# Optimization experiments

Hardware: AMD Instinct MI355X
Metric: run time of the kernel (lower is better)

The kernel has to match this reference:

```python
import jax, jax.numpy as jnp
import numpy as np

N = 50000          # nodes
E = 800000         # random edges (self-loops added in reference, per PyG default)
B = 64             # graphs in batch
IN_DIM = 773
HID = 256
OUT = 128
H1, D1 = 4, 64     # heads, head_dim layer 1 (256 = 4*64)
H2, D2 = 4, 32     # heads, head_dim layer 2 (128 = 4*32)
NEG_SLOPE = 0.2


def setup_inputs() -> dict:
    key = jax.random.key(0)
    ks = jax.random.split(key, 20)
    s = 0.02
    x = jax.random.normal(ks[0], (N, IN_DIM), dtype=jnp.float32)
    edge_index = jax.random.randint(ks[1], (2, E), 0, N, dtype=jnp.int32)
    batch = jnp.sort(jax.random.randint(ks[2], (N,), 0, B, dtype=jnp.int32))
    return {
        "x": x,
        "edge_index": edge_index,
        "batch": batch,
        "W_in": jax.random.normal(ks[3], (IN_DIM, HID), jnp.float32) * s,
        "b_in": jnp.zeros((HID,), jnp.float32),
        "W1": jax.random.normal(ks[4], (HID, H1 * D1), jnp.float32) * s,
        "att_src1": jax.random.normal(ks[5], (H1, D1), jnp.float32) * s,
        "att_dst1": jax.random.normal(ks[6], (H1, D1), jnp.float32) * s,
        "b1": jnp.zeros((H1 * D1,), jnp.float32),
        "W2": jax.random.normal(ks[7], (HID, H2 * D2), jnp.float32) * s,
        "att_src2": jax.random.normal(ks[8], (H2, D2), jnp.float32) * s,
        "att_dst2": jax.random.normal(ks[9], (H2, D2), jnp.float32) * s,
        "b2": jnp.zeros((H2 * D2,), jnp.float32),
        "W_cls": jax.random.normal(ks[10], (OUT, 2), jnp.float32) * s,
        "b_cls": jnp.zeros((2,), jnp.float32),
        "W_conf": jax.random.normal(ks[11], (OUT, 1), jnp.float32) * s,
        "b_conf": jnp.zeros((1,), jnp.float32),
    }


def _gat_layer(h, src, dst, W, att_src, att_dst, bias, heads, dim):
    # h: (N, F_in). PyG GATConv, concat=True, eval mode (dropout off).
    hW = (h @ W).reshape(N, heads, dim)                    # (N, H, D)
    a_src = jnp.einsum("nhd,hd->nh", hW, att_src)          # (N, H)
    a_dst = jnp.einsum("nhd,hd->nh", hW, att_dst)
    e = a_src[src] + a_dst[dst]                            # (E', H)
    e = jax.nn.leaky_relu(e, NEG_SLOPE)
    # segment softmax over incoming edges of each dst node
    m = jax.ops.segment_max(e, dst, num_segments=N)        # (N, H)
    ex = jnp.exp(e - m[dst])
    z = jax.ops.segment_sum(ex, dst, num_segments=N)       # (N, H)
    alpha = ex / (z[dst] + 1e-16)                          # (E', H)
    msg = hW[src] * alpha[:, :, None]                      # (E', H, D)
    out = jax.ops.segment_sum(msg, dst, num_segments=N)    # (N, H, D)
    return out.reshape(N, heads * dim) + bias


def reference(x, edge_index, batch, W_in, b_in,
              W1, att_src1, att_dst1, b1,
              W2, att_src2, att_dst2, b2,
              W_cls, b_cls, W_conf, b_conf):
    loops = jnp.arange(N, dtype=edge_index.dtype)
    src = jnp.concatenate([edge_index[0], loops])
    dst = jnp.concatenate([edge_index[1], loops])

    h = jax.nn.relu(x @ W_in + b_in)                       # (N, 256)
    h = jax.nn.relu(_gat_layer(h, src, dst, W1, att_src1, att_dst1, b1, H1, D1))
    h = _gat_layer(h, src, dst, W2, att_src2, att_dst2, b2, H2, D2)
    h = jax.nn.relu(h)                                     # (N, 128)

    # global mean pool over graphs
    sums = jax.ops.segment_sum(h, batch, num_segments=B)   # (B, 128)
    cnts = jax.ops.segment_sum(jnp.ones((N,), h.dtype), batch, num_segments=B)
    graph_emb = sums / jnp.maximum(cnts, 1.0)[:, None]

    class_logits = graph_emb @ W_cls + b_cls               # (B, 2)
    confidence = jax.nn.sigmoid(graph_emb @ W_conf + b_conf)  # (B, 1)
    return class_logits, confidence
```

## Files before the change

kernel.cpp:

```cpp
#include <hip/hip_runtime.h>
#include <math.h>

#define NN 50000
#define NE 800000
#define NB 64
#define IND 773
#define MPAD 50048
#define SCAN_B 196

typedef __attribute__((ext_vector_type(8))) short short8_t;
typedef __attribute__((ext_vector_type(4))) float f32x4;
typedef __attribute__((ext_vector_type(2))) float f32x2;

__device__ __forceinline__ float lrelu(float x) { return x > 0.f ? x : 0.2f * x; }
__device__ __forceinline__ short f2b(float f) {
    unsigned u = __float_as_uint(f);
    unsigned r = (u + 0x7fffu + ((u >> 16) & 1u)) >> 16;
    return (short)r;
}
__device__ __forceinline__ float b2f(short s) {
    return __uint_as_float(((unsigned)(unsigned short)s) << 16);
}
__device__ __forceinline__ unsigned char enc8(float v) {
    return (unsigned char)(__builtin_amdgcn_cvt_pk_fp8_f32(v, v, 0, false) & 0xff);
}
__device__ __forceinline__ void dec4(unsigned w, float* v) {
    f32x2 lo = __builtin_amdgcn_cvt_pk_f32_fp8((int)w, false);
    f32x2 hi = __builtin_amdgcn_cvt_pk_f32_fp8((int)w, true);
    v[0] = lo[0]; v[1] = lo[1]; v[2] = hi[0]; v[3] = hi[1];
}
__device__ __forceinline__ void dec2(unsigned w, float* v) {
    f32x2 lo = __builtin_amdgcn_cvt_pk_f32_fp8((int)w, false);
    v[0] = lo[0]; v[1] = lo[1];
}

#define GLOAD16(g, l) __builtin_amdgcn_global_load_lds(                         \
    (const __attribute__((address_space(1))) void*)(g),                         \
    (__attribute__((address_space(3))) void*)(l), 16, 0, 0)

__global__ __launch_bounds__(512) void gemm_a(const float* __restrict__ X,
                                              const short* __restrict__ Bt,
                                              const float* __restrict__ bias,
                                              short* __restrict__ C) {
    const int K = 800, N = 256, NT = 25;
    __shared__ short As[2][128 * 32];
    __shared__ short Bs[2][256 * 32];
    const int t = threadIdx.x;
    const int w = t >> 6, l = t & 63;
    const int l15 = l & 15, lh = l >> 4;
    const int bm = blockIdx.x * 128;
    const int wr = (w >> 2) * 64, wc = (w & 3) * 64;
    const int arow = t >> 2, acb = (t & 3) * 8;
    const int gm = bm + arow;
    const bool rowok = gm < NN;
    const float* xrow = X + (size_t)gm * IND;
    const short* bG = Bt + (size_t)(t >> 2) * K + (t & 3) * 8;

    f32x4 acc[4][4];
#pragma unroll
    for (int i = 0; i < 4; ++i)
#pragma unroll
        for (int j = 0; j < 4; ++j) acc[i][j] = (f32x4){0.f, 0.f, 0.f, 0.f};

    short8_t rA;
    auto loadA = [&](int it) {
        int gk = it * 32 + acb;
        if (rowok && gk + 7 < IND) {
            float4 v0 = *(const float4*)(xrow + gk);
            float4 v1 = *(const float4*)(xrow + gk + 4);
            rA[0] = f2b(v0.x); rA[1] = f2b(v0.y); rA[2] = f2b(v0.z); rA[3] = f2b(v0.w);
            rA[4] = f2b(v1.x); rA[5] = f2b(v1.y); rA[6] = f2b(v1.z); rA[7] = f2b(v1.w);
        } else {
#pragma unroll
            for (int j = 0; j < 8; ++j)
                rA[j] = (rowok && gk + j < IND) ? f2b(xrow[gk + j]) : (short)0;
        }
    };
    auto stageB = [&](int buf, int it) {
        GLOAD16(bG + it * 32, &Bs[buf][w * 512]);
        GLOAD16(bG + (size_t)128 * K + it * 32, &Bs[buf][128 * 32 + w * 512]);
    };

    loadA(0);
    stageB(0, 0);
    stageB(1, 1);
    *(short8_t*)&As[0][arow * 32 + acb] = rA;
    loadA(1);
    __syncthreads();

    for (int it = 0; it < NT; ++it) {
        const int c = it & 1, n = c ^ 1;
        short8_t af[4], bfr[4];
#pragma unroll
        for (int mi = 0; mi < 4; ++mi)
            af[mi] = *(const short8_t*)&As[c][(wr + mi * 16 + l15) * 32 + lh * 8];
#pragma unroll
        for (int ni = 0; ni < 4; ++ni)
            bfr[ni] = *(const short8_t*)&Bs[c][(wc + ni * 16 + l15) * 32 + lh * 8];
        if (it + 1 < NT) *(short8_t*)&As[n][arow * 32 + acb] = rA;
#pragma unroll
        for (int mi = 0; mi < 4; ++mi)
#pragma unroll
            for (int ni = 0; ni < 4; ++ni)
                acc[mi][ni] = __builtin_amdgcn_mfma_f32_16x16x32_bf16(af[mi], bfr[ni], acc[mi][ni], 0, 0, 0);
        __syncthreads();
        if (it + 2 < NT) {
            loadA(it + 2);
            stageB(c, it + 2);
        }
    }

#pragma unroll
    for (int mi = 0; mi < 4; ++mi) {
#pragma unroll
        for (int r = 0; r < 4; ++r) {
            int grow = bm + wr + mi * 16 + lh * 4 + r;
            if (grow >= NN) continue;
#pragma unroll
            for (int ni = 0; ni < 4; ++ni) {
                int gcol = wc + ni * 16 + l15;
                float v = fmaxf(acc[mi][ni][r] + bias[gcol], 0.f);
                C[(size_t)grow * N + gcol] = f2b(v);
            }
        }
    }
}

__global__ __launch_bounds__(256) void gemm_b(const short* __restrict__ A,
                                              const short* __restrict__ Bt,
                                              const float* __restrict__ att_s,
                                              const float* __restrict__ att_d,
                                              unsigned char* __restrict__ C8,
                                              float* __restrict__ a_s,
                                              float* __restrict__ a_d) {
    const int K = 256, N = 256, NT = 8;
    __shared__ short As[2][128 * 32];
    __shared__ short Bs[2][128 * 32];
    const int t = threadIdx.x;
    const int w = t >> 6, l = t & 63;
    const int l15 = l & 15, lh = l >> 4;
    const int bm = blockIdx.x * 128, bn = blockIdx.y * 128;
    const int wr = (w >> 1) * 64, wc = (w & 1) * 64;

    const short* aG = A + (size_t)(bm + w * 32 + (l >> 2)) * K + (l & 3) * 8;
    const short* bG = Bt + (size_t)(bn + w * 32 + (l >> 2)) * K + (l & 3) * 8;

    auto stage = [&](int buf, int k0) {
        GLOAD16(aG + k0, As[buf] + (w * 32) * 32);
        GLOAD16(aG + (size_t)16 * K + k0, As[buf] + (w * 32 + 16) * 32);
        GLOAD16(bG + k0, Bs[buf] + (w * 32) * 32);
        GLOAD16(bG + (size_t)16 * K + k0, Bs[buf] + (w * 32 + 16) * 32);
    };

    f32x4 acc[4][4];
#pragma unroll
    for (int i = 0; i < 4; ++i)
#pragma unroll
        for (int j = 0; j < 4; ++j) acc[i][j] = (f32x4){0.f, 0.f, 0.f, 0.f};

    stage(0, 0);
    stage(1, 32);
    __syncthreads();

    for (int it = 0; it < NT; ++it) {
        const int c = it & 1;
        short8_t af[4], bfr[4];
#pragma unroll
        for (int mi = 0; mi < 4; ++mi)
            af[mi] = *(const short8_t*)&As[c][(wr + mi * 16 + l15) * 32 + lh * 8];
#pragma unroll
        for (int ni = 0; ni < 4; ++ni)
            bfr[ni] = *(const short8_t*)&Bs[c][(wc + ni * 16 + l15) * 32 + lh * 8];
#pragma unroll
        for (int mi = 0; mi < 4; ++mi)
#pragma unroll
            for (int ni = 0; ni < 4; ++ni)
                acc[mi][ni] = __builtin_amdgcn_mfma_f32_16x16x32_bf16(af[mi], bfr[ni], acc[mi][ni], 0, 0, 0);
        __syncthreads();
        if (it + 2 < NT) stage(c, (it + 2) * 32);
    }

    const int head = (bn + wc) >> 6;
    float sa[4], sd[4];
#pragma unroll
    for (int ni = 0; ni < 4; ++ni) {
        sa[ni] = att_s[head * 64 + ni * 16 + l15];
        sd[ni] = att_d[head * 64 + ni * 16 + l15];
    }
    char* R = (char*)As;
#pragma unroll
    for (int mi = 0; mi < 4; ++mi) {
#pragma unroll
        for (int r = 0; r < 4; ++r) {
            int rloc = wr + mi * 16 + lh * 4 + r;
            int grow = bm + rloc;
            float s = acc[mi][0][r] * sa[0] + acc[mi][1][r] * sa[1] +
                      acc[mi][2][r] * sa[2] + acc[mi][3][r] * sa[3];
            float d = acc[mi][0][r] * sd[0] + acc[mi][1][r] * sd[1] +
                      acc[mi][2][r] * sd[2] + acc[mi][3][r] * sd[3];
#pragma unroll
            for (int off = 1; off < 16; off <<= 1) {
                s += __shfl_xor(s, off);
                d += __shfl_xor(d, off);
            }
            if (grow < NN && l15 == 0) { a_s[grow * 4 + head] = s; a_d[grow * 4 + head] = d; }
#pragma unroll
            for (int ni = 0; ni < 4; ++ni)
                R[rloc * 128 + wc + ni * 16 + l15] = (char)enc8(acc[mi][ni][r]);
        }
    }
    __syncthreads();
#pragma unroll
    for (int i = 0; i < 4; ++i) {
        int idx = i * 256 + t;
        int row = idx >> 3, cb = (idx & 7) * 16;
        int grow = bm + row;
        if (grow < NN)
            *(float4*)&C8[(size_t)grow * N + bn + cb] = *(float4*)&R[row * 128 + cb];
    }
}

__global__ __launch_bounds__(256) void gemm_c(const short* __restrict__ A,
                                              const short* __restrict__ Bt,
                                              const float* __restrict__ att_s,
                                              const float* __restrict__ att_d,
                                              unsigned char* __restrict__ C8,
                                              float* __restrict__ a_s,
                                              float* __restrict__ a_d) {
    const int K = 256, N = 128, NT = 8;
    __shared__ short As[2][128 * 32];
    __shared__ short Bs[2][128 * 32];
    const int t = threadIdx.x;
    const int w = t >> 6, l = t & 63;
    const int l15 = l & 15, lh = l >> 4;
    const int bm = blockIdx.x * 128;
    const int wr = (w >> 1) * 64, wc = (w & 1) * 64;

    const short* aG = A + (size_t)(bm + w * 32 + (l >> 2)) * K + (l & 3) * 8;
    const short* bG = Bt + (size_t)(w * 32 + (l >> 2)) * K + (l & 3) * 8;

    auto stage = [&](int buf, int k0) {
        GLOAD16(aG + k0, As[buf] + (w * 32) * 32);
        GLOAD16(aG + (size_t)16 * K + k0, As[buf] + (w * 32 + 16) * 32);
        GLOAD16(bG + k0, Bs[buf] + (w * 32) * 32);
        GLOAD16(bG + (size_t)16 * K + k0, Bs[buf] + (w * 32 + 16) * 32);
    };

    f32x4 acc[4][4];
#pragma unroll
    for (int i = 0; i < 4; ++i)
#pragma unroll
        for (int j = 0; j < 4; ++j) acc[i][j] = (f32x4){0.f, 0.f, 0.f, 0.f};

    stage(0, 0);
    stage(1, 32);
    __syncthreads();

    for (int it = 0; it < NT; ++it) {
        const int c = it & 1;
        short8_t af[4], bfr[4];
#pragma unroll
        for (int mi = 0; mi < 4; ++mi)
            af[mi] = *(const short8_t*)&As[c][(wr + mi * 16 + l15) * 32 + lh * 8];
#pragma unroll
        for (int ni = 0; ni < 4; ++ni)
            bfr[ni] = *(const short8_t*)&Bs[c][(wc + ni * 16 + l15) * 32 + lh * 8];
#pragma unroll
        for (int mi = 0; mi < 4; ++mi)
#pragma unroll
            for (int ni = 0; ni < 4; ++ni)
                acc[mi][ni] = __builtin_amdgcn_mfma_f32_16x16x32_bf16(af[mi], bfr[ni], acc[mi][ni], 0, 0, 0);
        __syncthreads();
        if (it + 2 < NT) stage(c, (it + 2) * 32);
    }

    const int h0 = wc >> 5;
    float sa[4], sd[4];
#pragma unroll
    for (int ni = 0; ni < 4; ++ni) {
        int idx = (h0 + (ni >> 1)) * 32 + (ni & 1) * 16 + l15;
        sa[ni] = att_s[idx];
        sd[ni] = att_d[idx];
    }
    char* R = (char*)As;
#pragma unroll
    for (int mi = 0; mi < 4; ++mi) {
#pragma unroll
        for (int r = 0; r < 4; ++r) {
            int rloc = wr + mi * 16 + lh * 4 + r;
            int grow = bm + rloc;
            float s0 = acc[mi][0][r] * sa[0] + acc[mi][1][r] * sa[1];
            float s1 = acc[mi][2][r] * sa[2] + acc[mi][3][r] * sa[3];
            float d0 = acc[mi][0][r] * sd[0] + acc[mi][1][r] * sd[1];
            float d1 = acc[mi][2][r] * sd[2] + acc[mi][3][r] * sd[3];
#pragma unroll
            for (int off = 1; off < 16; off <<= 1) {
                s0 += __shfl_xor(s0, off); s1 += __shfl_xor(s1, off);
                d0 += __shfl_xor(d0, off); d1 += __shfl_xor(d1, off);
            }
            if (grow < NN && l15 == 0) {
                a_s[grow * 4 + h0] = s0; a_s[grow * 4 + h0 + 1] = s1;
                a_d[grow * 4 + h0] = d0; a_d[grow * 4 + h0 + 1] = d1;
            }
#pragma unroll
            for (int ni = 0; ni < 4; ++ni)
                R[rloc * 128 + wc + ni * 16 + l15] = (char)enc8(acc[mi][ni][r]);
        }
    }
    __syncthreads();
#pragma unroll
    for (int i = 0; i < 4; ++i) {
        int idx = i * 256 + t;
        int row = idx >> 3, cb = (idx & 7) * 16;
        int grow = bm + row;
        if (grow < NN)
            *(float4*)&C8[(size_t)grow * N + cb] = *(float4*)&R[row * 128 + cb];
    }
}

__global__ __launch_bounds__(256) void k_prep(const float* __restrict__ W_in,
                                              const float* __restrict__ W1,
                                              const float* __restrict__ W2,
                                              short* __restrict__ Wt_in,
                                              short* __restrict__ Wt1,
                                              short* __restrict__ Wt2,
                                              int* __restrict__ deg) {
    int b = blockIdx.x;
    const float* W; short* Wt; int K, N, Kp, kb, nb;
    if (b < 200)      { W = W_in; Wt = Wt_in; K = IND; N = 256; Kp = 800; kb = (b % 25) * 32; nb = (b / 25) * 32; }
    else if (b < 264) { b -= 200; W = W1; Wt = Wt1; K = 256; N = 256; Kp = 256; kb = (b % 8) * 32; nb = (b / 8) * 32; }
    else if (b < 296) { b -= 264; W = W2; Wt = Wt2; K = 256; N = 128; Kp = 256; kb = (b % 8) * 32; nb = (b / 8) * 32; }
    else {
        int i = (b - 296) * 256 + threadIdx.x;
        if (i < NN) deg[i] = 0;
        return;
    }
    __shared__ short tile[32][33];
    int tx = threadIdx.x & 31, ty = threadIdx.x >> 5;
#pragma unroll
    for (int r = 0; r < 32; r += 8) {
        int k = kb + ty + r;
        tile[ty + r][tx] = (k < K) ? f2b(W[(size_t)k * N + nb + tx]) : (short)0;
    }
    __syncthreads();
#pragma unroll
    for (int r = 0; r < 32; r += 8) {
        int n = nb + ty + r, k = kb + tx;
        Wt[(size_t)n * Kp + k] = tile[tx][ty + r];
    }
}

__global__ void k_hist(const int* __restrict__ ei, int* __restrict__ deg) {
    int e = blockIdx.x * 256 + threadIdx.x;
    if (e >= NE) return;
    atomicAdd(&deg[ei[NE + e]], 1);
}

__global__ __launch_bounds__(256) void k_bsum(const int* __restrict__ deg,
                                              int* __restrict__ bsum) {
    int i = blockIdx.x * 256 + threadIdx.x;
    int v = (i < NN) ? deg[i] : 0;
#pragma unroll
    for (int off = 32; off; off >>= 1) v += __shfl_down(v, off);
    __shared__ int ws[4];
    if ((threadIdx.x & 63) == 0) ws[threadIdx.x >> 6] = v;
    __syncthreads();
    if (threadIdx.x == 0) bsum[blockIdx.x] = ws[0] + ws[1] + ws[2] + ws[3];
}

__global__ __launch_bounds__(256) void k_scan3(const int* __restrict__ deg,
                                               const int* __restrict__ bsum,
                                               int* __restrict__ rowp,
                                               int* __restrict__ cursor) {
    int b = blockIdx.x;
    int i = b * 256 + threadIdx.x;
    int d = (i < NN) ? deg[i] : 0;
    __shared__ int sb[SCAN_B];
    if (threadIdx.x < SCAN_B) sb[threadIdx.x] = bsum[threadIdx.x];
    int v = d;
    int lane = threadIdx.x & 63, wid = threadIdx.x >> 6;
#pragma unroll
    for (int off = 1; off < 64; off <<= 1) {
        int u = __shfl_up(v, off);
        if (lane >= off) v += u;
    }
    __shared__ int ws[4];
    if (lane == 63) ws[wid] = v;
    __syncthreads();
    int add = 0;
    for (int q = 0; q < b; ++q) add += sb[q];
    for (int wq = 0; wq < wid; ++wq) add += ws[wq];
    int excl = add + v - d;
    if (i < NN) { rowp[i] = excl; cursor[i] = excl; }
    if (i == NN - 1) rowp[NN] = excl + d;
}

__global__ void k_scatter(const int* __restrict__ ei, int* __restrict__ cursor,
                          int* __restrict__ colidx) {
    int e = blockIdx.x * 256 + threadIdx.x;
    if (e >= NE) return;
    int s = ei[e], d = ei[NE + e];
    int pos = atomicAdd(&cursor[d], 1);
    colidx[pos] = s;
}

template<int HD>
__global__ __launch_bounds__(256) void gat_agg(const unsigned char* __restrict__ hW8,
                                               const float* __restrict__ a_s,
                                               const float* __restrict__ a_d,
                                               const int* __restrict__ row_ptr,
                                               const int* __restrict__ colidx,
                                               const float* __restrict__ bias,
                                               short* __restrict__ outp) {
    const int CPL = HD / 64;
    int node = blockIdx.x * 4 + (threadIdx.x >> 6);
    int lane = threadIdx.x & 63;
    if (node >= NN) return;
    int h = lane >> 4;
    int start = row_ptr[node], end = row_ptr[node + 1];
    float adst = a_d[node * 4 + h];
    float eself = lrelu(a_s[node * 4 + h] + adst);

    float z = 1.f;
    float acc[CPL];
    {
        const unsigned char* row = hW8 + (size_t)node * HD + lane * CPL;
        if (CPL == 4) dec4(*(const unsigned*)row, acc);
        else          dec2(*(const unsigned short*)row, acc);
    }
    for (int e = start; e < end; e += 8) {
        int sidx[8];
        float xs[8], ex[8];
#pragma unroll
        for (int q = 0; q < 8; ++q) {
            int ee = e + q;
            sidx[q] = colidx[ee < end ? ee : end - 1];
        }
#pragma unroll
        for (int q = 0; q < 8; ++q) xs[q] = a_s[sidx[q] * 4 + h];
        float v[8][CPL];
        if (CPL == 4) {
#pragma unroll
            for (int q = 0; q < 8; ++q)
                dec4(*(const unsigned*)(hW8 + (size_t)sidx[q] * HD + lane * 4), v[q]);
        } else {
#pragma unroll
            for (int q = 0; q < 8; ++q)
                dec2(*(const unsigned short*)(hW8 + (size_t)sidx[q] * HD + lane * 2), v[q]);
        }
#pragma unroll
        for (int q = 0; q < 8; ++q) {
            float wq = __expf(lrelu(xs[q] + adst) - eself);
            ex[q] = (e + q < end) ? wq : 0.f;
        }
#pragma unroll
        for (int q = 0; q < 8; ++q) z += ex[q];
#pragma unroll
        for (int j = 0; j < CPL; ++j) {
            float a = 0.f;
#pragma unroll
            for (int q = 0; q < 8; ++q) a += ex[q] * v[q][j];
            acc[j] += a;
        }
    }
    float inv = 1.f / z;
    short* orow = outp + (size_t)node * HD + lane * CPL;
#pragma unroll
    for (int j = 0; j < CPL; ++j)
        orow[j] = f2b(fmaxf(acc[j] * inv + bias[lane * CPL + j], 0.f));
}

__global__ __launch_bounds__(512) void pool_head(const short* __restrict__ h2,
                                                 const int* __restrict__ batch,
                                                 const float* __restrict__ W_cls,
                                                 const float* __restrict__ b_cls,
                                                 const float* __restrict__ W_conf,
                                                 const float* __restrict__ b_conf,
                                                 float* __restrict__ out) {
    int b = blockIdx.x;
    int t = threadIdx.x & 127;
    int g = threadIdx.x >> 7;
    int lo = 0, hi = NN;
    while (lo < hi) { int mid = (lo + hi) >> 1; if (batch[mid] < b) lo = mid + 1; else hi = mid; }
    int start = lo;
    lo = 0; hi = NN;
    while (lo < hi) { int mid = (lo + hi) >> 1; if (batch[mid] < b + 1) lo = mid + 1; else hi = mid; }
    int end = lo;

    float acc = 0.f;
    for (int n = start + g; n < end; n += 4) acc += b2f(h2[(size_t)n * 128 + t]);
    __shared__ float se[4][128];
    se[g][t] = acc;
    __syncthreads();
    if (g == 0) {
        float emb = (se[0][t] + se[1][t] + se[2][t] + se[3][t]) /
                    fmaxf((float)(end - start), 1.f);
        se[0][t] = emb;
    }
    __syncthreads();
    if (threadIdx.x == 0) {
        float v = b_cls[0];
        for (int c = 0; c < 128; ++c) v += se[0][c] * W_cls[c * 2 + 0];
        out[b * 2 + 0] = v;
    } else if (threadIdx.x == 1) {
        float v = b_cls[1];
        for (int c = 0; c < 128; ++c) v += se[0][c] * W_cls[c * 2 + 1];
        out[b * 2 + 1] = v;
    } else if (threadIdx.x == 2) {
        float v = b_conf[0];
        for (int c = 0; c < 128; ++c) v += se[0][c] * W_conf[c];
        out[128 + b] = 1.f / (1.f + expf(-v));
    }
}

extern "C" void kernel_launch(void* const* d_in, const int* in_sizes, int n_in,
                              void* d_out, int out_size, void* d_ws, size_t ws_size,
                              hipStream_t stream) {
    const float* x        = (const float*)d_in[0];
    const int*   ei       = (const int*)d_in[1];
    const int*   batch    = (const int*)d_in[2];
    const float* W_in     = (const float*)d_in[3];
    const float* b_in     = (const float*)d_in[4];
    const float* W1       = (const float*)d_in[5];
    const float* att_src1 = (const float*)d_in[6];
    const float* att_dst1 = (const float*)d_in[7];
    const float* b1       = (const float*)d_in[8];
    const float* W2       = (const float*)d_in[9];
    const float* att_src2 = (const float*)d_in[10];
    const float* att_dst2 = (const float*)d_in[11];
    const float* b2       = (const float*)d_in[12];
    const float* W_cls    = (const float*)d_in[13];
    const float* b_cls    = (const float*)d_in[14];
    const float* W_conf   = (const float*)d_in[15];
    const float* b_conf   = (const float*)d_in[16];
    float* out = (float*)d_out;

    char* ws = (char*)d_ws;
    short*         h0   = (short*)(ws + 0);
    unsigned char* hW1  = (unsigned char*)(ws + 25624576);
    short*         h1   = (short*)(ws + 38436864);
    unsigned char* hW2  = (unsigned char*)(ws + 64061440);
    short*         h2   = (short*)(ws + 70467584);
    size_t base = 83279872;
    short* Wt_in = (short*)(ws + base);
    short* Wt1   = (short*)(ws + base + 409600);
    short* Wt2   = (short*)(ws + base + 540672);
    float* a_s1  = (float*)(ws + base + 606208);
    float* a_d1  = (float*)(ws + base + 1406208);
    int*   deg    = (int*)(ws + base + 2206208);
    int*   rowp   = (int*)(ws + base + 2406208);
    int*   cursor = (int*)(ws + base + 2606272);
    int*   colidx = (int*)(ws + base + 2806272);
    int*   bsum   = (int*)(ws + base + 6006272);

    k_prep<<<296 + SCAN_B, 256, 0, stream>>>(W_in, W1, W2, Wt_in, Wt1, Wt2, deg);
    k_hist<<<NE / 256, 256, 0, stream>>>(ei, deg);
    k_bsum<<<SCAN_B, 256, 0, stream>>>(deg, bsum);
    k_scan3<<<SCAN_B, 256, 0, stream>>>(deg, bsum, rowp, cursor);
    k_scatter<<<NE / 256, 256, 0, stream>>>(ei, cursor, colidx);

    gemm_a<<<391, 512, 0, stream>>>(x, Wt_in, b_in, h0);
    gemm_b<<<dim3(391, 2), 256, 0, stream>>>(h0, Wt1, att_src1, att_dst1, hW1, a_s1, a_d1);
    gat_agg<256><<<12500, 256, 0, stream>>>(hW1, a_s1, a_d1, rowp, colidx, b1, h1);
    gemm_c<<<391, 256, 0, stream>>>(h1, Wt2, att_src2, att_dst2, hW2, a_s1, a_d1);
    gat_agg<128><<<12500, 256, 0, stream>>>(hW2, a_s1, a_d1, rowp, colidx, b2, h2);
    pool_head<<<NB, 512, 0, stream>>>(h2, batch, W_cls, b_cls, W_conf, b_conf, out);
}
```

Baseline: 347.0 us.

## Store intermediate activations and weights in FP8 and use FP8 MFMA for hidden GEMMs

gemm_a and the first GAT aggregation now write their activations as FP8 instead of bf16. gemm_b and gemm_c run fp8 x fp8 MFMA, reading FP8 operands and FP8-transposed weights, which halves the bytes staged through LDS. Mean pooling is also split across 4x more blocks with atomic accumulation, followed by a separate small head kernel. The aim is to cut memory traffic for the large N x 256 intermediates and GEMM operand loads, at the cost of lower precision (FP8 inputs to the matmuls) and an extra kernel launch.

New measurement: 343.5 us, median of 3. About the same (-1.0%).

```diff
diff --git a/kernel.cpp b/kernel.cpp
--- a/kernel.cpp
+++ b/kernel.cpp
@@ -24,6 +24,12 @@
 __device__ __forceinline__ unsigned char enc8(float v) {
     return (unsigned char)(__builtin_amdgcn_cvt_pk_fp8_f32(v, v, 0, false) & 0xff);
 }
+__device__ __forceinline__ unsigned pack4fp8(float a, float b, float c, float d) {
+    unsigned w = 0;
+    w = __builtin_amdgcn_cvt_pk_fp8_f32(a, b, w, false);
+    w = __builtin_amdgcn_cvt_pk_fp8_f32(c, d, w, true);
+    return w;
+}
 __device__ __forceinline__ void dec4(unsigned w, float* v) {
     f32x2 lo = __builtin_amdgcn_cvt_pk_f32_fp8((int)w, false);
     f32x2 hi = __builtin_amdgcn_cvt_pk_f32_fp8((int)w, true);
@@ -41,7 +47,7 @@
 __global__ __launch_bounds__(512) void gemm_a(const float* __restrict__ X,
                                               const short* __restrict__ Bt,
                                               const float* __restrict__ bias,
-                                              short* __restrict__ C) {
+                                              unsigned char* __restrict__ C8) {
     const int K = 800, N = 256, NT = 25;
     __shared__ short As[2][128 * 32];
     __shared__ short Bs[2][256 * 32];
@@ -110,46 +116,52 @@
         }
     }
 
+    char* R = (char*)Bs;
 #pragma unroll
     for (int mi = 0; mi < 4; ++mi) {
 #pragma unroll
         for (int r = 0; r < 4; ++r) {
-            int grow = bm + wr + mi * 16 + lh * 4 + r;
-            if (grow >= NN) continue;
+            int rloc = wr + mi * 16 + lh * 4 + r;
 #pragma unroll
             for (int ni = 0; ni < 4; ++ni) {
                 int gcol = wc + ni * 16 + l15;
                 float v = fmaxf(acc[mi][ni][r] + bias[gcol], 0.f);
-                C[(size_t)grow * N + gcol] = f2b(v);
+                R[rloc * 256 + gcol] = (char)enc8(v);
             }
         }
     }
-}
-
-__global__ __launch_bounds__(256) void gemm_b(const short* __restrict__ A,
-                                              const short* __restrict__ Bt,
+    __syncthreads();
+#pragma unroll
+    for (int i = 0; i < 4; ++i) {
+        int idx = i * 512 + t;
+        int row = idx >> 4, cb = (idx & 15) * 16;
+        int grow = bm + row;
+        if (grow < NN)
+            *(float4*)&C8[(size_t)grow * N + cb] = *(float4*)&R[row * 256 + cb];
+    }
+}
+
+__global__ __launch_bounds__(256) void gemm_b(const unsigned char* __restrict__ A8,
+                                              const unsigned char* __restrict__ B8,
                                               const float* __restrict__ att_s,
                                               const float* __restrict__ att_d,
                                               unsigned char* __restrict__ C8,
                                               float* __restrict__ a_s,
                                               float* __restrict__ a_d) {
     const int K = 256, N = 256, NT = 8;
-    __shared__ short As[2][128 * 32];
-    __shared__ short Bs[2][128 * 32];
+    __shared__ char LDS8[16384];
     const int t = threadIdx.x;
     const int w = t >> 6, l = t & 63;
     const int l15 = l & 15, lh = l >> 4;
     const int bm = blockIdx.x * 128, bn = blockIdx.y * 128;
     const int wr = (w >> 1) * 64, wc = (w & 1) * 64;
 
-    const short* aG = A + (size_t)(bm + w * 32 + (l >> 2)) * K + (l & 3) * 8;
-    const short* bG = Bt + (size_t)(bn + w * 32 + (l >> 2)) * K + (l & 3) * 8;
+    const unsigned char* aG = A8 + (size_t)(bm + w * 32 + (l >> 1)) * K + (l & 1) * 16;
+    const unsigned char* bG = B8 + (size_t)(bn + w * 32 + (l >> 1)) * K + (l & 1) * 16;
 
     auto stage = [&](int buf, int k0) {
-        GLOAD16(aG + k0, As[buf] + (w * 32) * 32);
-        GLOAD16(aG + (size_t)16 * K + k0, As[buf] + (w * 32 + 16) * 32);
-        GLOAD16(bG + k0, Bs[buf] + (w * 32) * 32);
-        GLOAD16(bG + (size_t)16 * K + k0, Bs[buf] + (w * 32 + 16) * 32);
+        GLOAD16(aG + k0, LDS8 + buf * 4096 + w * 1024);
+        GLOAD16(bG + k0, LDS8 + 8192 + buf * 4096 + w * 1024);
     };
 
     f32x4 acc[4][4];
@@ -164,18 +176,18 @@
 
     for (int it = 0; it < NT; ++it) {
         const int c = it & 1;
-        short8_t af[4], bfr[4];
+        long af[4], bfr[4];
 #pragma unroll
         for (int mi = 0; mi < 4; ++mi)
-            af[mi] = *(const short8_t*)&As[c][(wr + mi * 16 + l15) * 32 + lh * 8];
+            af[mi] = *(const long*)&LDS8[c * 4096 + (wr + mi * 16 + l15) * 32 + lh * 8];
 #pragma unroll
         for (int ni = 0; ni < 4; ++ni)
-            bfr[ni] = *(const short8_t*)&Bs[c][(wc + ni * 16 + l15) * 32 + lh * 8];
+            bfr[ni] = *(const long*)&LDS8[8192 + c * 4096 + (wc + ni * 16 + l15) * 32 + lh * 8];
 #pragma unroll
         for (int mi = 0; mi < 4; ++mi)
 #pragma unroll
             for (int ni = 0; ni < 4; ++ni)
-                acc[mi][ni] = __builtin_amdgcn_mfma_f32_16x16x32_bf16(af[mi], bfr[ni], acc[mi][ni], 0, 0, 0);
+                acc[mi][ni] = __builtin_amdgcn_mfma_f32_16x16x32_fp8_fp8(af[mi], bfr[ni], acc[mi][ni], 0, 0, 0);
         __syncthreads();
         if (it + 2 < NT) stage(c, (it + 2) * 32);
     }
@@ -187,7 +199,7 @@
         sa[ni] = att_s[head * 64 + ni * 16 + l15];
         sd[ni] = att_d[head * 64 + ni * 16 + l15];
     }
-    char* R = (char*)As;
+    char* R = LDS8;
 #pragma unroll
     for (int mi = 0; mi < 4; ++mi) {
 #pragma unroll
@@ -220,30 +232,27 @@
     }
 }
 
-__global__ __launch_bounds__(256) void gemm_c(const short* __restrict__ A,
-                                              const short* __restrict__ Bt,
+__global__ __launch_bounds__(256) void gemm_c(const unsigned char* __restrict__ A8,
+                                              const unsigned char* __restrict__ B8,
                                               const float* __restrict__ att_s,
                                               const float* __restrict__ att_d,
                                               unsigned char* __restrict__ C8,
                                               float* __restrict__ a_s,
                                               float* __restrict__ a_d) {
     const int K = 256, N = 128, NT = 8;
-    __shared__ short As[2][128 * 32];
-    __shared__ short Bs[2][128 * 32];
+    __shared__ char LDS8[16384];
     const int t = threadIdx.x;
     const int w = t >> 6, l = t & 63;
     const int l15 = l & 15, lh = l >> 4;
     const int bm = blockIdx.x * 128;
     const int wr = (w >> 1) * 64, wc = (w & 1) * 64;
 
-    const short* aG = A + (size_t)(bm + w * 32 + (l >> 2)) * K + (l & 3) * 8;
-    const short* bG = Bt + (size_t)(w * 32 + (l >> 2)) * K + (l & 3) * 8;
+    const unsigned char* aG = A8 + (size_t)(bm + w * 32 + (l >> 1)) * K + (l & 1) * 16;
+    const unsigned char* bG = B8 + (size_t)(w * 32 + (l >> 1)) * K + (l & 1) * 16;
 
     auto stage = [&](int buf, int k0) {
-        GLOAD16(aG + k0, As[buf] + (w * 32) * 32);
-        GLOAD16(aG + (size_t)16 * K + k0, As[buf] + (w * 32 + 16) * 32);
-        GLOAD16(bG + k0, Bs[buf] + (w * 32) * 32);
-        GLOAD16(bG + (size_t)16 * K + k0, Bs[buf] + (w * 32 + 16) * 32);
+        GLOAD16(aG + k0, LDS8 + buf * 4096 + w * 1024);
+        GLOAD16(bG + k0, LDS8 + 8192 + buf * 4096 + w * 1024);
     };
 
     f32x4 acc[4][4];
@@ -258,18 +267,18 @@
 
     for (int it = 0; it < NT; ++it) {
         const int c = it & 1;
-        short8_t af[4], bfr[4];
+        long af[4], bfr[4];
 #pragma unroll
         for (int mi = 0; mi < 4; ++mi)
-            af[mi] = *(const short8_t*)&As[c][(wr + mi * 16 + l15) * 32 + lh * 8];
+            af[mi] = *(const long*)&LDS8[c * 4096 + (wr + mi * 16 + l15) * 32 + lh * 8];
 #pragma unroll
         for (int ni = 0; ni < 4; ++ni)
-            bfr[ni] = *(const short8_t*)&Bs[c][(wc + ni * 16 + l15) * 32 + lh * 8];
+            bfr[ni] = *(const long*)&LDS8[8192 + c * 4096 + (wc + ni * 16 + l15) * 32 + lh * 8];
 #pragma unroll
         for (int mi = 0; mi < 4; ++mi)
 #pragma unroll
             for (int ni = 0; ni < 4; ++ni)
-                acc[mi][ni] = __builtin_amdgcn_mfma_f32_16x16x32_bf16(af[mi], bfr[ni], acc[mi][ni], 0, 0, 0);
+                acc[mi][ni] = __builtin_amdgcn_mfma_f32_16x16x32_fp8_fp8(af[mi], bfr[ni], acc[mi][ni], 0, 0, 0);
         __syncthreads();
         if (it + 2 < NT) stage(c, (it + 2) * 32);
     }
@@ -282,7 +291,7 @@
         sa[ni] = att_s[idx];
         sd[ni] = att_d[idx];
     }
-    char* R = (char*)As;
+    char* R = LDS8;
 #pragma unroll
     for (int mi = 0; mi < 4; ++mi) {
 #pragma unroll
@@ -322,31 +331,36 @@
                                               const float* __restrict__ W1,
                                               const float* __restrict__ W2,
                                               short* __restrict__ Wt_in,
-                                              short* __restrict__ Wt1,
-                                              short* __restrict__ Wt2,
-                                              int* __restrict__ deg) {
+                                              unsigned char* __restrict__ Wt1,
+                                              unsigned char* __restrict__ Wt2,
+                                              int* __restrict__ deg,
+                                              float* __restrict__ emb) {
     int b = blockIdx.x;
-    const float* W; short* Wt; int K, N, Kp, kb, nb;
-    if (b < 200)      { W = W_in; Wt = Wt_in; K = IND; N = 256; Kp = 800; kb = (b % 25) * 32; nb = (b / 25) * 32; }
-    else if (b < 264) { b -= 200; W = W1; Wt = Wt1; K = 256; N = 256; Kp = 256; kb = (b % 8) * 32; nb = (b / 8) * 32; }
-    else if (b < 296) { b -= 264; W = W2; Wt = Wt2; K = 256; N = 128; Kp = 256; kb = (b % 8) * 32; nb = (b / 8) * 32; }
+    const float* W; int K, N, Kp, kb, nb, fp8;
+    short* Wts = nullptr; unsigned char* Wt8 = nullptr;
+    if (b < 200)      { W = W_in; Wts = Wt_in; fp8 = 0; K = IND; N = 256; Kp = 800; kb = (b % 25) * 32; nb = (b / 25) * 32; }
+    else if (b < 264) { b -= 200; W = W1; Wt8 = Wt1; fp8 = 1; K = 256; N = 256; Kp = 256; kb = (b % 8) * 32; nb = (b / 8) * 32; }
+    else if (b < 296) { b -= 264; W = W2; Wt8 = Wt2; fp8 = 1; K = 256; N = 128; Kp = 256; kb = (b % 8) * 32; nb = (b / 8) * 32; }
     else {
         int i = (b - 296) * 256 + threadIdx.x;
         if (i < NN) deg[i] = 0;
+        if (i < NB * 128) emb[i] = 0.f;
         return;
     }
-    __shared__ short tile[32][33];
+    __shared__ float tile[32][33];
     int tx = threadIdx.x & 31, ty = threadIdx.x >> 5;
 #pragma unroll
     for (int r = 0; r < 32; r += 8) {
         int k = kb + ty + r;
-        tile[ty + r][tx] = (k < K) ? f2b(W[(size_t)k * N + nb + tx]) : (short)0;
+        tile[ty + r][tx] = (k < K) ? W[(size_t)k * N + nb + tx] : 0.f;
     }
     __syncthreads();
 #pragma unroll
     for (int r = 0; r < 32; r += 8) {
         int n = nb + ty + r, k = kb + tx;
-        Wt[(size_t)n * Kp + k] = tile[tx][ty + r];
+        float v = tile[tx][ty + r];
+        if (fp8) Wt8[(size_t)n * Kp + k] = enc8(v);
+        else     Wts[(size_t)n * Kp + k] = f2b(v);
     }
 }
 
@@ -404,14 +418,14 @@
     colidx[pos] = s;
 }
 
-template<int HD>
+template<int HD, int OUT8>
 __global__ __launch_bounds__(256) void gat_agg(const unsigned char* __restrict__ hW8,
                                                const float* __restrict__ a_s,
                                                const float* __restrict__ a_d,
                                                const int* __restrict__ row_ptr,
                                                const int* __restrict__ colidx,
                                                const float* __restrict__ bias,
-                                               short* __restrict__ outp) {
+                                               void* __restrict__ outp) {
     const int CPL = HD / 64;
     int node = blockIdx.x * 4 + (threadIdx.x >> 6);
     int lane = threadIdx.x & 63;
@@ -464,51 +478,66 @@
         }
     }
     float inv = 1.f / z;
-    short* orow = outp + (size_t)node * HD + lane * CPL;
+    float o[CPL];
 #pragma unroll
     for (int j = 0; j < CPL; ++j)
-        orow[j] = f2b(fmaxf(acc[j] * inv + bias[lane * CPL + j], 0.f));
-}
-
-__global__ __launch_bounds__(512) void pool_head(const short* __restrict__ h2,
-                                                 const int* __restrict__ batch,
-                                                 const float* __restrict__ W_cls,
-                                                 const float* __restrict__ b_cls,
-                                                 const float* __restrict__ W_conf,
-                                                 const float* __restrict__ b_conf,
-                                                 float* __restrict__ out) {
-    int b = blockIdx.x;
-    int t = threadIdx.x & 127;
-    int g = threadIdx.x >> 7;
+        o[j] = fmaxf(acc[j] * inv + bias[lane * CPL + j], 0.f);
+    if (OUT8) {
+        unsigned* orow = (unsigned*)((unsigned char*)outp + (size_t)node * HD + lane * 4);
+        *orow = pack4fp8(o[0], o[1], (CPL == 4 ? o[2] : 0.f), (CPL == 4 ? o[3] : 0.f));
+    } else {
+        short* orow = (short*)outp + (size_t)node * HD + lane * CPL;
+#pragma unroll
+        for (int j = 0; j < CPL; ++j) orow[j] = f2b(o[j]);
+    }
+}
+
+__global__ __launch_bounds__(128) void k_pool(const short* __restrict__ h2,
+                                              const int* __restrict__ batch,
+                                              float* __restrict__ emb) {
+    int b = blockIdx.x >> 2;
+    int chunk = blockIdx.x & 3;
+    int t = threadIdx.x;
     int lo = 0, hi = NN;
     while (lo < hi) { int mid = (lo + hi) >> 1; if (batch[mid] < b) lo = mid + 1; else hi = mid; }
     int start = lo;
     lo = 0; hi = NN;
     while (lo < hi) { int mid = (lo + hi) >> 1; if (batch[mid] < b + 1) lo = mid + 1; else hi = mid; }
     int end = lo;
-
-    float acc = 0.f;
-    for (int n = start + g; n < end; n += 4) acc += b2f(h2[(size_t)n * 128 + t]);
-    __shared__ float se[4][128];
-    se[g][t] = acc;
-    __syncthreads();
-    if (g == 0) {
-        float emb = (se[0][t] + se[1][t] + se[2][t] + se[3][t]) /
-                    fmaxf((float)(end - start), 1.f);
-        se[0][t] = emb;
-    }
-    __syncthreads();
-    if (threadIdx.x == 0) {
+    float s = 0.f;
+    for (int n = start + chunk; n < end; n += 4) s += b2f(h2[(size_t)n * 128 + t]);
+    atomicAdd(&emb[b * 128 + t], s);
+}
+
+__global__ __launch_bounds__(128) void k_head(const float* __restrict__ emb,
+                                              const int* __restrict__ batch,
+                                              const float* __restrict__ W_cls,
+                                              const float* __restrict__ b_cls,
+                                              const float* __restrict__ W_conf,
+                                              const float* __restrict__ b_conf,
+                                              float* __restrict__ out) {
+    int b = blockIdx.x;
+    int t = threadIdx.x;
+    int lo = 0, hi = NN;
+    while (lo < hi) { int mid = (lo + hi) >> 1; if (batch[mid] < b) lo = mid + 1; else hi = mid; }
+    int start = lo;
+    lo = 0; hi = NN;
+    while (lo < hi) { int mid = (lo + hi) >> 1; if (batch[mid] < b + 1) lo = mid + 1; else hi = mid; }
+    int end = lo;
+    __shared__ float se[128];
+    se[t] = emb[b * 128 + t] / fmaxf((float)(end - start), 1.f);
+    __syncthreads();
+    if (t == 0) {
         float v = b_cls[0];
-        for (int c = 0; c < 128; ++c) v += se[0][c] * W_cls[c * 2 + 0];
+        for (int c = 0; c < 128; ++c) v += se[c] * W_cls[c * 2 + 0];
         out[b * 2 + 0] = v;
-    } else if (threadIdx.x == 1) {
+    } else if (t == 1) {
         float v = b_cls[1];
-        for (int c = 0; c < 128; ++c) v += se[0][c] * W_cls[c * 2 + 1];
+        for (int c = 0; c < 128; ++c) v += se[c] * W_cls[c * 2 + 1];
         out[b * 2 + 1] = v;
-    } else if (threadIdx.x == 2) {
+    } else if (t == 2) {
         float v = b_conf[0];
-        for (int c = 0; c < 128; ++c) v += se[0][c] * W_conf[c];
+        for (int c = 0; c < 128; ++c) v += se[c] * W_conf[c];
         out[128 + b] = 1.f / (1.f + expf(-v));
     }
 }
@@ -536,24 +565,25 @@
     float* out = (float*)d_out;
 
     char* ws = (char*)d_ws;
-    short*         h0   = (short*)(ws + 0);
-    unsigned char* hW1  = (unsigned char*)(ws + 25624576);
-    short*         h1   = (short*)(ws + 38436864);
-    unsigned char* hW2  = (unsigned char*)(ws + 64061440);
-    short*         h2   = (short*)(ws + 70467584);
-    size_t base = 83279872;
-    short* Wt_in = (short*)(ws + base);
-    short* Wt1   = (short*)(ws + base + 409600);
-    short* Wt2   = (short*)(ws + base + 540672);
-    float* a_s1  = (float*)(ws + base + 606208);
-    float* a_d1  = (float*)(ws + base + 1406208);
-    int*   deg    = (int*)(ws + base + 2206208);
-    int*   rowp   = (int*)(ws + base + 2406208);
-    int*   cursor = (int*)(ws + base + 2606272);
-    int*   colidx = (int*)(ws + base + 2806272);
-    int*   bsum   = (int*)(ws + base + 6006272);
-
-    k_prep<<<296 + SCAN_B, 256, 0, stream>>>(W_in, W1, W2, Wt_in, Wt1, Wt2, deg);
+    unsigned char* h0  = (unsigned char*)(ws + 0);
+    unsigned char* hW1 = (unsigned char*)(ws + 12812288);
+    unsigned char* h1  = (unsigned char*)(ws + 25624576);
+    unsigned char* hW2 = (unsigned char*)(ws + 38436864);
+    short*         h2  = (short*)(ws + 44843008);
+    size_t base = 57655296;
+    short*         Wt_in = (short*)(ws + base);
+    unsigned char* Wt1   = (unsigned char*)(ws + base + 409600);
+    unsigned char* Wt2   = (unsigned char*)(ws + base + 475136);
+    float* a_s1  = (float*)(ws + base + 507904);
+    float* a_d1  = (float*)(ws + base + 1307904);
+    float* emb   = (float*)(ws + base + 2107904);
+    int*   deg    = (int*)(ws + base + 2140672);
+    int*   rowp   = (int*)(ws + base + 2340672);
+    int*   cursor = (int*)(ws + base + 2540736);
+    int*   colidx = (int*)(ws + base + 2740736);
+    int*   bsum   = (int*)(ws + base + 5940736);
+
+    k_prep<<<296 + SCAN_B, 256, 0, stream>>>(W_in, W1, W2, Wt_in, Wt1, Wt2, deg, emb);
     k_hist<<<NE / 256, 256, 0, stream>>>(ei, deg);
     k_bsum<<<SCAN_B, 256, 0, stream>>>(deg, bsum);
     k_scan3<<<SCAN_B, 256, 0, stream>>>(deg, bsum, rowp, cursor);
@@ -561,8 +591,9 @@
 
     gemm_a<<<391, 512, 0, stream>>>(x, Wt_in, b_in, h0);
     gemm_b<<<dim3(391, 2), 256, 0, stream>>>(h0, Wt1, att_src1, att_dst1, hW1, a_s1, a_d1);
-    gat_agg<256><<<12500, 256, 0, stream>>>(hW1, a_s1, a_d1, rowp, colidx, b1, h1);
+    gat_agg<256, 1><<<12500, 256, 0, stream>>>(hW1, a_s1, a_d1, rowp, colidx, b1, h1);
     gemm_c<<<391, 256, 0, stream>>>(h1, Wt2, att_src2, att_dst2, hW2, a_s1, a_d1);
-    gat_agg<128><<<12500, 256, 0, stream>>>(hW2, a_s1, a_d1, rowp, colidx, b2, h2);
-    pool_head<<<NB, 512, 0, stream>>>(h2, batch, W_cls, b_cls, W_conf, b_conf, out);
-}
+    gat_agg<128, 0><<<12500, 256, 0, stream>>>(hW2, a_s1, a_d1, rowp, colidx, b2, h2);
+    k_pool<<<NB * 4, 128, 0, stream>>>(h2, batch, emb);
+    k_head<<<NB, 128, 0, stream>>>(emb, batch, W_cls, b_cls, W_conf, b_conf, out);
+}
```
